# Optimization experiments

Hardware: AMD Instinct MI355X
Metric: run time of the kernel (lower is better)

The kernel has to match this reference:

```python
import jax, jax.numpy as jnp
import numpy as np


def setup_inputs() -> dict:
    key = jax.random.key(0)
    k1, k2, k3, k4 = jax.random.split(key, 4)
    B, IN, OUT, R = 4096, 4096, 4096, 256
    x = jax.random.normal(k1, (B, IN), dtype=jnp.float32)
    U = jax.random.normal(k2, (R, IN), dtype=jnp.float32) / np.sqrt(IN)
    V = jax.random.normal(k3, (OUT, R), dtype=jnp.float32) / np.sqrt(R)
    bias = jax.random.uniform(k4, (OUT,), dtype=jnp.float32,
                              minval=-IN ** -0.5, maxval=IN ** -0.5)
    return {"x": x, "U": U, "V": V, "bias": bias}


def reference(x, U, V, bias):
    # Low-rank linear: out[b,j] = sum_k V[j,k] * (sum_i U[k,i] * x[b,i]) + bias[j]
    # (the torch loops with sparsity=1.0 / keep_stride==1 compute exactly this)
    t = jnp.einsum('bi,ri->br', x, U)        # [B, R]
    out = jnp.einsum('br,or->bo', t, V) + bias  # [B, OUT]
    return out
```

## Files before the change

### kernel.cpp

```cpp
#include <hip/hip_runtime.h>

typedef __attribute__((ext_vector_type(8))) short bf16x8;
typedef __attribute__((ext_vector_type(4))) float f32x4;

__device__ __forceinline__ unsigned short f2bf(float f) {
  unsigned int u = __float_as_uint(f);
  return (unsigned short)((u + 0x7fffu + ((u >> 16) & 1u)) >> 16);
}

__device__ __forceinline__ float bf2f(unsigned short s) {
  return __uint_as_float(((unsigned int)s) << 16);
}

__device__ __forceinline__ unsigned int cvtpk(float a, float b) {
  unsigned int w;
  asm("v_cvt_pk_bf16_f32 %0, %1, %2" : "=v"(w) : "v"(a), "v"(b));
  return w;
}

__device__ __forceinline__ void gload_lds16(const void* g, void* l) {
  __builtin_amdgcn_global_load_lds((const __attribute__((address_space(1))) void*)g,
                                   (__attribute__((address_space(3))) void*)l,
                                   16, 0, 0);
}

__global__ void castUV(const float4* __restrict__ U, const float4* __restrict__ V,
                       ushort4* __restrict__ Ub, ushort4* __restrict__ Vb) {
  const int NU = 256 * 4096 / 4;
  int i = blockIdx.x * 256 + threadIdx.x;
  const float4* s; ushort4* d; int j;
  if (i < NU) { s = U; d = Ub; j = i; }
  else        { s = V; d = Vb; j = i - NU; }
  float4 v = s[j];
  ushort4 o;
  o.x = f2bf(v.x); o.y = f2bf(v.y); o.z = f2bf(v.z); o.w = f2bf(v.w);
  d[j] = o;
}

__global__ __launch_bounds__(256)
void gemm1_f32a(const float* __restrict__ x, const unsigned short* __restrict__ Ub,
                unsigned short* __restrict__ P) {
  __shared__ __align__(16) float sA[2][64 * 32];
  __shared__ __align__(16) unsigned short sB[2][256 * 32];

  const int tid = threadIdx.x;
  const int l = tid & 63;
  const int w = tid >> 6;
  const int wn = w * 64;
  const int rm = blockIdx.x * 64;
  const int k0base = blockIdx.z * 256;
  const int lr = l & 15;
  const int lg = l >> 4;

  auto stage = [&](int kt, int buf) {
    const int k0 = k0base + kt * 32;
#pragma unroll
    for (int is = 0; is < 4; ++is) {
      int s = is * 256 + tid;
      int r = s >> 2;
      gload_lds16(Ub + (long long)r * 4096 + k0 + 8 * ((s & 3) ^ (r & 3)),
                  (char*)sB[buf] + s * 16);
    }
#pragma unroll
    for (int is = 0; is < 2; ++is) {
      int s = is * 256 + tid;
      int r = s >> 3;
      gload_lds16(x + (long long)(rm + r) * 4096 + k0 + 4 * ((s & 7) ^ (r & 7)),
                  (char*)sA[buf] + s * 16);
    }
  };

  f32x4 acc[4][4] = {};

  stage(0, 0);
  for (int kt = 0; kt < 8; ++kt) {
    __syncthreads();
    if (kt < 7) stage(kt + 1, (kt + 1) & 1);
    const char* a0 = (const char*)sA[kt & 1];
    const char* b0 = (const char*)sB[kt & 1];
    bf16x8 af[4], bfr[4];
#pragma unroll
    for (int m = 0; m < 4; ++m) {
      const int row = m * 16 + lr;
      const int byte0 = row * 128 + ((lg * 32) ^ ((row & 7) << 4));
      float4 f0 = *(const float4*)(a0 + byte0);
      float4 f1 = *(const float4*)(a0 + (byte0 ^ 16));
      unsigned int w0 = cvtpk(f0.x, f0.y), w1 = cvtpk(f0.z, f0.w);
      unsigned int w2 = cvtpk(f1.x, f1.y), w3 = cvtpk(f1.z, f1.w);
      uint4 packed = {w0, w1, w2, w3};
      af[m] = __builtin_bit_cast(bf16x8, packed);
    }
#pragma unroll
    for (int n = 0; n < 4; ++n) {
      const int row = wn + n * 16 + lr;
      bfr[n] = *(const bf16x8*)(b0 + row * 64 + ((lg * 16) ^ ((row & 3) << 4)));
    }
#pragma unroll
    for (int m = 0; m < 4; ++m)
#pragma unroll
      for (int n = 0; n < 4; ++n)
        acc[m][n] = __builtin_amdgcn_mfma_f32_16x16x32_bf16(af[m], bfr[n], acc[m][n], 0, 0, 0);
  }

  unsigned short* Pz = P + (long long)blockIdx.z * (4096LL * 256);
  const int r0 = rm + lg * 4;
#pragma unroll
  for (int n = 0; n < 4; ++n) {
    const int cc = wn + n * 16 + lr;
#pragma unroll
    for (int m = 0; m < 4; ++m)
#pragma unroll
      for (int i = 0; i < 4; ++i)
        Pz[(long long)(r0 + m * 16 + i) * 256 + cc] = f2bf(acc[m][n][i]);
  }
}

__global__ void reduce16(const ushort4* __restrict__ P, ushort4* __restrict__ t) {
  const int S = 4096 * 256 / 4;
  int i = blockIdx.x * 256 + threadIdx.x;
  float sx = 0, sy = 0, sz = 0, sw = 0;
#pragma unroll
  for (int z = 0; z < 16; ++z) {
    ushort4 v = P[i + z * S];
    sx += bf2f(v.x); sy += bf2f(v.y); sz += bf2f(v.z); sw += bf2f(v.w);
  }
  ushort4 o;
  o.x = f2bf(sx); o.y = f2bf(sy); o.z = f2bf(sz); o.w = f2bf(sw);
  t[i] = o;
}

__global__ __launch_bounds__(256)
void gemm2(const unsigned short* __restrict__ A,
           const unsigned short* __restrict__ B,
           const float* __restrict__ bias,
           float* __restrict__ C) {
  __shared__ __align__(16) unsigned short sA[2][128 * 32];
  __shared__ __align__(16) unsigned short sB[2][128 * 32];

  const int tid = threadIdx.x;
  const int l = tid & 63;
  const int w = tid >> 6;
  const int wm = (w >> 1) * 64;
  const int wn = (w & 1) * 64;
  const int rm = blockIdx.x * 128;
  const int rn = blockIdx.y * 128;
  const int lr = l & 15;
  const int lg = l >> 4;

  auto stage = [&](int kt, int buf) {
    const int k0 = kt * 32;
#pragma unroll
    for (int is = 0; is < 2; ++is) {
      int s = is * 256 + tid;
      int r = s >> 2;
      gload_lds16(B + (long long)(rn + r) * 256 + k0 + 8 * ((s & 3) ^ (r & 3)),
                  (char*)sB[buf] + s * 16);
    }
#pragma unroll
    for (int is = 0; is < 2; ++is) {
      int s = is * 256 + tid;
      int r = s >> 2;
      gload_lds16(A + (long long)(rm + r) * 256 + k0 + 8 * ((s & 3) ^ (r & 3)),
                  (char*)sA[buf] + s * 16);
    }
  };

  f32x4 acc[4][4] = {};

  stage(0, 0);
  for (int kt = 0; kt < 8; ++kt) {
    __syncthreads();
    if (kt < 7) stage(kt + 1, (kt + 1) & 1);
    const char* a0 = (const char*)sA[kt & 1];
    const char* b0 = (const char*)sB[kt & 1];
    bf16x8 af[4], bfr[4];
#pragma unroll
    for (int m = 0; m < 4; ++m) {
      const int row = wm + m * 16 + lr;
      af[m] = *(const bf16x8*)(a0 + row * 64 + ((lg * 16) ^ ((row & 3) << 4)));
    }
#pragma unroll
    for (int n = 0; n < 4; ++n) {
      const int row = wn + n * 16 + lr;
      bfr[n] = *(const bf16x8*)(b0 + row * 64 + ((lg * 16) ^ ((row & 3) << 4)));
    }
#pragma unroll
    for (int m = 0; m < 4; ++m)
#pragma unroll
      for (int n = 0; n < 4; ++n)
        acc[m][n] = __builtin_amdgcn_mfma_f32_16x16x32_bf16(af[m], bfr[n], acc[m][n], 0, 0, 0);
  }

  const int r0 = rm + wm + lg * 4;
  const int c0 = rn + wn + lr;
#pragma unroll
  for (int n = 0; n < 4; ++n) {
    const int cc = c0 + n * 16;
    const float badd = bias[cc];
#pragma unroll
    for (int m = 0; m < 4; ++m)
#pragma unroll
      for (int i = 0; i < 4; ++i)
        C[(long long)(r0 + m * 16 + i) * 4096 + cc] = acc[m][n][i] + badd;
  }
}

extern "C" void kernel_launch(void* const* d_in, const int* in_sizes, int n_in,
                              void* d_out, int out_size, void* d_ws, size_t ws_size,
                              hipStream_t stream) {
  const float* x    = (const float*)d_in[0];
  const float* U    = (const float*)d_in[1];
  const float* V    = (const float*)d_in[2];
  const float* bias = (const float*)d_in[3];
  float* out = (float*)d_out;

  char* ws = (char*)d_ws;
  unsigned short* P   = (unsigned short*)ws;
  unsigned short* tb  = (unsigned short*)(ws + (32u << 20));
  unsigned short* Ub  = (unsigned short*)(ws + (34u << 20));
  unsigned short* Vb  = (unsigned short*)(ws + (36u << 20));

  castUV<<<2048, 256, 0, stream>>>((const float4*)U, (const float4*)V,
                                   (ushort4*)Ub, (ushort4*)Vb);

  dim3 g1(64, 1, 16);
  gemm1_f32a<<<g1, 256, 0, stream>>>(x, Ub, P);

  reduce16<<<1024, 256, 0, stream>>>((const ushort4*)P, (ushort4*)tb);

  dim3 g2(32, 32, 1);
  gemm2<<<g2, 256, 0, stream>>>(tb, Vb, bias, out);
}
```

Before: 63.82 us.

## Pre-pack U into MFMA fragment layout and drop LDS staging in gemm1

The prep kernel now writes U in bf16, reordered so that each lane's MFMA B fragment is one contiguous 16-byte load. gemm1 drops LDS and barriers entirely. Each wave reads x straight from global memory into registers with a two-deep prefetch and reads the packed U fragments directly, computing a 32x256 tile per wave. Blocks cover 128 rows each, so the grid halves. This removes the LDS traffic and synchronisation. In exchange it puts heavy register pressure on 32 accumulators per lane and relies on L2 to serve the U fragments that all blocks reread.

```diff
diff --git a/kernel.cpp b/kernel.cpp
--- a/kernel.cpp
+++ b/kernel.cpp
@@ -24,94 +24,94 @@
                                    16, 0, 0);
 }
 
-__global__ void castUV(const float4* __restrict__ U, const float4* __restrict__ V,
-                       ushort4* __restrict__ Ub, ushort4* __restrict__ Vb) {
-  const int NU = 256 * 4096 / 4;
+__global__ void prep(const float* __restrict__ U, const float4* __restrict__ V,
+                     unsigned short* __restrict__ Upk, ushort4* __restrict__ Vb) {
   int i = blockIdx.x * 256 + threadIdx.x;
-  const float4* s; ushort4* d; int j;
-  if (i < NU) { s = U; d = Ub; j = i; }
-  else        { s = V; d = Vb; j = i - NU; }
-  float4 v = s[j];
-  ushort4 o;
-  o.x = f2bf(v.x); o.y = f2bf(v.y); o.z = f2bf(v.z); o.w = f2bf(v.w);
-  d[j] = o;
-}
-
-__global__ __launch_bounds__(256)
-void gemm1_f32a(const float* __restrict__ x, const unsigned short* __restrict__ Ub,
-                unsigned short* __restrict__ P) {
-  __shared__ __align__(16) float sA[2][64 * 32];
-  __shared__ __align__(16) unsigned short sB[2][256 * 32];
-
+  const int NUP = 128 * 16 * 64;
+  if (i < NUP) {
+    int l = i & 63, n = (i >> 6) & 15, jg = i >> 10;
+    const float* src = U + (long long)(n * 16 + (l & 15)) * 4096 + jg * 32 + (l >> 4) * 8;
+    float4 a = *(const float4*)src;
+    float4 b = *(const float4*)(src + 4);
+    ushort4 o0, o1;
+    o0.x = f2bf(a.x); o0.y = f2bf(a.y); o0.z = f2bf(a.z); o0.w = f2bf(a.w);
+    o1.x = f2bf(b.x); o1.y = f2bf(b.y); o1.z = f2bf(b.z); o1.w = f2bf(b.w);
+    ushort4* d = (ushort4*)(Upk + (long long)i * 8);
+    d[0] = o0; d[1] = o1;
+  } else {
+    int j = i - NUP;
+    float4 v = V[j];
+    ushort4 o;
+    o.x = f2bf(v.x); o.y = f2bf(v.y); o.z = f2bf(v.z); o.w = f2bf(v.w);
+    Vb[j] = o;
+  }
+}
+
+__global__ __launch_bounds__(256, 2)
+void gemm1_direct(const float* __restrict__ x, const unsigned short* __restrict__ Upk,
+                  unsigned short* __restrict__ P) {
   const int tid = threadIdx.x;
   const int l = tid & 63;
   const int w = tid >> 6;
-  const int wn = w * 64;
-  const int rm = blockIdx.x * 64;
-  const int k0base = blockIdx.z * 256;
+  const int mg = blockIdx.x;
+  const int z = blockIdx.z;
   const int lr = l & 15;
   const int lg = l >> 4;
 
-  auto stage = [&](int kt, int buf) {
-    const int k0 = k0base + kt * 32;
-#pragma unroll
-    for (int is = 0; is < 4; ++is) {
-      int s = is * 256 + tid;
-      int r = s >> 2;
-      gload_lds16(Ub + (long long)r * 4096 + k0 + 8 * ((s & 3) ^ (r & 3)),
-                  (char*)sB[buf] + s * 16);
-    }
-#pragma unroll
-    for (int is = 0; is < 2; ++is) {
-      int s = is * 256 + tid;
-      int r = s >> 3;
-      gload_lds16(x + (long long)(rm + r) * 4096 + k0 + 4 * ((s & 7) ^ (r & 7)),
-                  (char*)sA[buf] + s * 16);
-    }
-  };
-
-  f32x4 acc[4][4] = {};
-
-  stage(0, 0);
-  for (int kt = 0; kt < 8; ++kt) {
-    __syncthreads();
-    if (kt < 7) stage(kt + 1, (kt + 1) & 1);
-    const char* a0 = (const char*)sA[kt & 1];
-    const char* b0 = (const char*)sB[kt & 1];
-    bf16x8 af[4], bfr[4];
-#pragma unroll
-    for (int m = 0; m < 4; ++m) {
-      const int row = m * 16 + lr;
-      const int byte0 = row * 128 + ((lg * 32) ^ ((row & 7) << 4));
-      float4 f0 = *(const float4*)(a0 + byte0);
-      float4 f1 = *(const float4*)(a0 + (byte0 ^ 16));
-      unsigned int w0 = cvtpk(f0.x, f0.y), w1 = cvtpk(f0.z, f0.w);
-      unsigned int w2 = cvtpk(f1.x, f1.y), w3 = cvtpk(f1.z, f1.w);
-      uint4 packed = {w0, w1, w2, w3};
-      af[m] = __builtin_bit_cast(bf16x8, packed);
-    }
-#pragma unroll
-    for (int n = 0; n < 4; ++n) {
-      const int row = wn + n * 16 + lr;
-      bfr[n] = *(const bf16x8*)(b0 + row * 64 + ((lg * 16) ^ ((row & 3) << 4)));
-    }
-#pragma unroll
-    for (int m = 0; m < 4; ++m)
-#pragma unroll
-      for (int n = 0; n < 4; ++n)
-        acc[m][n] = __builtin_amdgcn_mfma_f32_16x16x32_bf16(af[m], bfr[n], acc[m][n], 0, 0, 0);
-  }
-
-  unsigned short* Pz = P + (long long)blockIdx.z * (4096LL * 256);
-  const int r0 = rm + lg * 4;
-#pragma unroll
-  for (int n = 0; n < 4; ++n) {
-    const int cc = wn + n * 16 + lr;
-#pragma unroll
-    for (int m = 0; m < 4; ++m)
-#pragma unroll
-      for (int i = 0; i < 4; ++i)
-        Pz[(long long)(r0 + m * 16 + i) * 256 + cc] = f2bf(acc[m][n][i]);
+  const float* xb = x + (long long)(mg * 128 + w * 32 + lr) * 4096 + z * 256 + lg * 8;
+  const unsigned short* uz = Upk + ((long long)(z * 8) * 16 * 64 + l) * 8;
+
+  float4 xr[2][4];
+
+#define XPRE(J, S)                                            \
+  {                                                           \
+    const float* p0_ = xb + (J) * 32;                         \
+    const float* p1_ = p0_ + 16 * 4096;                       \
+    xr[S][0] = *(const float4*)p0_;                           \
+    xr[S][1] = *(const float4*)(p0_ + 4);                     \
+    xr[S][2] = *(const float4*)p1_;                           \
+    xr[S][3] = *(const float4*)(p1_ + 4);                     \
+  }
+
+  f32x4 acc0[16] = {};
+  f32x4 acc1[16] = {};
+
+  XPRE(0, 0);
+  XPRE(1, 1);
+
+#pragma unroll
+  for (int j = 0; j < 8; ++j) {
+    float4 a0 = xr[j & 1][0], a1 = xr[j & 1][1];
+    float4 a2 = xr[j & 1][2], a3 = xr[j & 1][3];
+    if (j + 2 < 8) XPRE(j + 2, (j + 2) & 1);
+    unsigned int w0 = cvtpk(a0.x, a0.y), w1 = cvtpk(a0.z, a0.w);
+    unsigned int w2 = cvtpk(a1.x, a1.y), w3 = cvtpk(a1.z, a1.w);
+    uint4 pk0 = {w0, w1, w2, w3};
+    bf16x8 af0 = __builtin_bit_cast(bf16x8, pk0);
+    unsigned int w4 = cvtpk(a2.x, a2.y), w5 = cvtpk(a2.z, a2.w);
+    unsigned int w6 = cvtpk(a3.x, a3.y), w7 = cvtpk(a3.z, a3.w);
+    uint4 pk1 = {w4, w5, w6, w7};
+    bf16x8 af1 = __builtin_bit_cast(bf16x8, pk1);
+    const unsigned short* uj = uz + j * 16 * 512;
+#pragma unroll
+    for (int n = 0; n < 16; ++n) {
+      bf16x8 b = *(const bf16x8*)(uj + n * 512);
+      acc0[n] = __builtin_amdgcn_mfma_f32_16x16x32_bf16(af0, b, acc0[n], 0, 0, 0);
+      acc1[n] = __builtin_amdgcn_mfma_f32_16x16x32_bf16(af1, b, acc1[n], 0, 0, 0);
+    }
+  }
+#undef XPRE
+
+  unsigned short* Pz = P + (long long)z * (4096LL * 256);
+  const int r0 = mg * 128 + w * 32 + lg * 4;
+#pragma unroll
+  for (int n = 0; n < 16; ++n) {
+    const int cc = n * 16 + lr;
+#pragma unroll
+    for (int i = 0; i < 4; ++i) {
+      Pz[(long long)(r0 + i) * 256 + cc] = f2bf(acc0[n][i]);
+      Pz[(long long)(r0 + 16 + i) * 256 + cc] = f2bf(acc1[n][i]);
+    }
   }
 }
 
@@ -217,14 +217,13 @@
   char* ws = (char*)d_ws;
   unsigned short* P   = (unsigned short*)ws;
   unsigned short* tb  = (unsigned short*)(ws + (32u << 20));
-  unsigned short* Ub  = (unsigned short*)(ws + (34u << 20));
+  unsigned short* Upk = (unsigned short*)(ws + (34u << 20));
   unsigned short* Vb  = (unsigned short*)(ws + (36u << 20));
 
-  castUV<<<2048, 256, 0, stream>>>((const float4*)U, (const float4*)V,
-                                   (ushort4*)Ub, (ushort4*)Vb);
-
-  dim3 g1(64, 1, 16);
-  gemm1_f32a<<<g1, 256, 0, stream>>>(x, Ub, P);
+  prep<<<1536, 256, 0, stream>>>(U, (const float4*)V, Upk, (ushort4*)Vb);
+
+  dim3 g1(32, 1, 16);
+  gemm1_direct<<<g1, 256, 0, stream>>>(x, Upk, P);
 
   reduce16<<<1024, 256, 0, stream>>>((const ushort4*)P, (ushort4*)tb);
 
```

Result: slower. 74.53 us (+16.8%).

## Pre-cast x to bf16 and halve split-K partitions in first GEMM

Applied to the files above, without the earlier changes.

Adds a grid-stride prep kernel that casts x along with U and V to bf16, so gemm1 stages bf16 A tiles instead of fp32 and skips the in-loop packing conversion. Split-K drops from 16 to 8 slices of 512 each, which halves the partial-sum buffer and the reduction reads. The cost is an extra full read of x plus a write of its bf16 copy in the prep pass, and gemm1 now runs only 512 blocks, which lowers parallelism.

```diff
diff --git a/kernel.cpp b/kernel.cpp
--- a/kernel.cpp
+++ b/kernel.cpp
@@ -10,12 +10,6 @@
 
 __device__ __forceinline__ float bf2f(unsigned short s) {
   return __uint_as_float(((unsigned int)s) << 16);
-}
-
-__device__ __forceinline__ unsigned int cvtpk(float a, float b) {
-  unsigned int w;
-  asm("v_cvt_pk_bf16_f32 %0, %1, %2" : "=v"(w) : "v"(a), "v"(b));
-  return w;
 }
 
 __device__ __forceinline__ void gload_lds16(const void* g, void* l) {
@@ -24,23 +18,30 @@
                                    16, 0, 0);
 }
 
-__global__ void castUV(const float4* __restrict__ U, const float4* __restrict__ V,
-                       ushort4* __restrict__ Ub, ushort4* __restrict__ Vb) {
+__global__ void prep(const float4* __restrict__ x, const float4* __restrict__ U,
+                     const float4* __restrict__ V, ushort4* __restrict__ xb,
+                     ushort4* __restrict__ Ub, ushort4* __restrict__ Vb) {
+  const int NX = 4096 * 4096 / 4;
   const int NU = 256 * 4096 / 4;
   int i = blockIdx.x * 256 + threadIdx.x;
-  const float4* s; ushort4* d; int j;
-  if (i < NU) { s = U; d = Ub; j = i; }
-  else        { s = V; d = Vb; j = i - NU; }
-  float4 v = s[j];
-  ushort4 o;
-  o.x = f2bf(v.x); o.y = f2bf(v.y); o.z = f2bf(v.z); o.w = f2bf(v.w);
-  d[j] = o;
+  const int stride = gridDim.x * 256;
+  for (; i < NX + 2 * NU; i += stride) {
+    const float4* s; ushort4* d; int j;
+    if (i < NX)           { s = x; d = xb; j = i; }
+    else if (i < NX + NU) { s = U; d = Ub; j = i - NX; }
+    else                  { s = V; d = Vb; j = i - NX - NU; }
+    float4 v = s[j];
+    ushort4 o;
+    o.x = f2bf(v.x); o.y = f2bf(v.y); o.z = f2bf(v.z); o.w = f2bf(v.w);
+    d[j] = o;
+  }
 }
 
 __global__ __launch_bounds__(256)
-void gemm1_f32a(const float* __restrict__ x, const unsigned short* __restrict__ Ub,
+void gemm1_bf16(const unsigned short* __restrict__ A,
+                const unsigned short* __restrict__ B,
                 unsigned short* __restrict__ P) {
-  __shared__ __align__(16) float sA[2][64 * 32];
+  __shared__ __align__(16) unsigned short sA[2][64 * 32];
   __shared__ __align__(16) unsigned short sB[2][256 * 32];
 
   const int tid = threadIdx.x;
@@ -48,7 +49,7 @@
   const int w = tid >> 6;
   const int wn = w * 64;
   const int rm = blockIdx.x * 64;
-  const int k0base = blockIdx.z * 256;
+  const int k0base = blockIdx.z * 512;
   const int lr = l & 15;
   const int lg = l >> 4;
 
@@ -58,14 +59,13 @@
     for (int is = 0; is < 4; ++is) {
       int s = is * 256 + tid;
       int r = s >> 2;
-      gload_lds16(Ub + (long long)r * 4096 + k0 + 8 * ((s & 3) ^ (r & 3)),
+      gload_lds16(B + (long long)r * 4096 + k0 + 8 * ((s & 3) ^ (r & 3)),
                   (char*)sB[buf] + s * 16);
     }
-#pragma unroll
-    for (int is = 0; is < 2; ++is) {
-      int s = is * 256 + tid;
-      int r = s >> 3;
-      gload_lds16(x + (long long)(rm + r) * 4096 + k0 + 4 * ((s & 7) ^ (r & 7)),
+    {
+      int s = tid;
+      int r = s >> 2;
+      gload_lds16(A + (long long)(rm + r) * 4096 + k0 + 8 * ((s & 3) ^ (r & 3)),
                   (char*)sA[buf] + s * 16);
     }
   };
@@ -73,22 +73,16 @@
   f32x4 acc[4][4] = {};
 
   stage(0, 0);
-  for (int kt = 0; kt < 8; ++kt) {
+  for (int kt = 0; kt < 16; ++kt) {
     __syncthreads();
-    if (kt < 7) stage(kt + 1, (kt + 1) & 1);
+    if (kt < 15) stage(kt + 1, (kt + 1) & 1);
     const char* a0 = (const char*)sA[kt & 1];
     const char* b0 = (const char*)sB[kt & 1];
     bf16x8 af[4], bfr[4];
 #pragma unroll
     for (int m = 0; m < 4; ++m) {
       const int row = m * 16 + lr;
-      const int byte0 = row * 128 + ((lg * 32) ^ ((row & 7) << 4));
-      float4 f0 = *(const float4*)(a0 + byte0);
-      float4 f1 = *(const float4*)(a0 + (byte0 ^ 16));
-      unsigned int w0 = cvtpk(f0.x, f0.y), w1 = cvtpk(f0.z, f0.w);
-      unsigned int w2 = cvtpk(f1.x, f1.y), w3 = cvtpk(f1.z, f1.w);
-      uint4 packed = {w0, w1, w2, w3};
-      af[m] = __builtin_bit_cast(bf16x8, packed);
+      af[m] = *(const bf16x8*)(a0 + row * 64 + ((lg * 16) ^ ((row & 3) << 4)));
     }
 #pragma unroll
     for (int n = 0; n < 4; ++n) {
@@ -115,12 +109,12 @@
   }
 }
 
-__global__ void reduce16(const ushort4* __restrict__ P, ushort4* __restrict__ t) {
+__global__ void reduce8(const ushort4* __restrict__ P, ushort4* __restrict__ t) {
   const int S = 4096 * 256 / 4;
   int i = blockIdx.x * 256 + threadIdx.x;
   float sx = 0, sy = 0, sz = 0, sw = 0;
 #pragma unroll
-  for (int z = 0; z < 16; ++z) {
+  for (int z = 0; z < 8; ++z) {
     ushort4 v = P[i + z * S];
     sx += bf2f(v.x); sy += bf2f(v.y); sz += bf2f(v.z); sw += bf2f(v.w);
   }
@@ -216,17 +210,18 @@
 
   char* ws = (char*)d_ws;
   unsigned short* P   = (unsigned short*)ws;
-  unsigned short* tb  = (unsigned short*)(ws + (32u << 20));
-  unsigned short* Ub  = (unsigned short*)(ws + (34u << 20));
-  unsigned short* Vb  = (unsigned short*)(ws + (36u << 20));
-
-  castUV<<<2048, 256, 0, stream>>>((const float4*)U, (const float4*)V,
-                                   (ushort4*)Ub, (ushort4*)Vb);
-
-  dim3 g1(64, 1, 16);
-  gemm1_f32a<<<g1, 256, 0, stream>>>(x, Ub, P);
-
-  reduce16<<<1024, 256, 0, stream>>>((const ushort4*)P, (ushort4*)tb);
+  unsigned short* tb  = (unsigned short*)(ws + (16u << 20));
+  unsigned short* Ub  = (unsigned short*)(ws + (18u << 20));
+  unsigned short* Vb  = (unsigned short*)(ws + (20u << 20));
+  unsigned short* xb  = (unsigned short*)(ws + (22u << 20));
+
+  prep<<<2048, 256, 0, stream>>>((const float4*)x, (const float4*)U, (const float4*)V,
+                                 (ushort4*)xb, (ushort4*)Ub, (ushort4*)Vb);
+
+  dim3 g1(64, 1, 8);
+  gemm1_bf16<<<g1, 256, 0, stream>>>(xb, Ub, P);
+
+  reduce8<<<1024, 256, 0, stream>>>((const ushort4*)P, (ushort4*)tb);
 
   dim3 g2(32, 32, 1);
   gemm2<<<g2, 256, 0, stream>>>(tb, Vb, bias, out);
```

After: 65.15 us. 1.02x slower.
